# Performance work log

Measured on AMD Instinct MI355X. Metric: run time of the kernel, lower is better.

## Reference

```python
import jax, jax.numpy as jnp
import numpy as np

NUM_HEADS = 12

def setup_inputs() -> dict:
    key = jax.random.key(0)
    ks = jax.random.split(key, 6)
    B, N, C = 4, 2048, 768
    s = 0.02
    return {
        "x": jax.random.normal(ks[0], (B, N, C), jnp.float32),
        "y": jax.random.normal(ks[1], (B, N, C), jnp.float32),
        "Wq": jax.random.normal(ks[2], (C, C), jnp.float32) * s,
        "Wkv": jax.random.normal(ks[3], (2 * C, C), jnp.float32) * s,
        "tau_param": jnp.asarray(1.0, jnp.float32),
        "Wproj": jax.random.normal(ks[4], (C, C), jnp.float32) * s,
        "bproj": jnp.zeros((C,), jnp.float32),
    }

def reference(x, y, Wq, Wkv, tau_param, Wproj, bproj):
    B, N, C = x.shape
    H = NUM_HEADS
    D = C // H
    scale = D ** -0.5
    # q: [B,H,N,D]
    q = (x @ Wq.T).reshape(B, N, H, D).transpose(0, 2, 1, 3) * scale
    kv = (y @ Wkv.T).reshape(B, N, 2, H, D).transpose(2, 0, 3, 1, 4)
    k, v = kv[0], kv[1]
    tau = jax.nn.softplus(tau_param) + 1e-6
    attn = jnp.einsum("bhnd,bhmd->bhnm", q, k) / tau  # [B,H,N,N]
    attn = jax.nn.softmax(attn, axis=-1)
    out = jnp.einsum("bhnm,bhmd->bhnd", attn, v)  # [B,H,N,D]
    out = out.transpose(0, 2, 1, 3).reshape(B, N, C)
    return out @ Wproj.T + bproj
```

## Files before the change

### kernel.cpp

```cpp
#include <hip/hip_runtime.h>
#include <math.h>

typedef unsigned short u16;
typedef unsigned int u32;
typedef __fp16 fp16x2 __attribute__((ext_vector_type(2)));
typedef _Float16 half8 __attribute__((ext_vector_type(8)));
typedef float f32x4 __attribute__((ext_vector_type(4)));

#define NH   12
#define SEQ  2048
#define CDIM 768

__device__ __forceinline__ u16 f2h(float f) {
  _Float16 h = (_Float16)f;
  return __builtin_bit_cast(u16, h);
}
__device__ __forceinline__ u32 pk2(float a, float b) {
  fp16x2 h = __builtin_amdgcn_cvt_pkrtz(a, b);
  return __builtin_bit_cast(u32, h);
}
__device__ __forceinline__ void dma16(const u16* g, u16* l) {
  __builtin_amdgcn_global_load_lds(
      (const __attribute__((address_space(1))) u32*)g,
      (__attribute__((address_space(3))) u32*)l, 16, 0, 0);
}

__global__ __launch_bounds__(256) void cvt_f32_f16(const float* __restrict__ in,
                                                   u16* __restrict__ out, int n) {
  int i = (blockIdx.x * 256 + threadIdx.x) * 4;
  if (i < n) {
    float4 f = *(const float4*)(in + i);
    *(uint2*)(out + i) = make_uint2(pk2(f.x, f.y), pk2(f.z, f.w));
  }
}
__global__ __launch_bounds__(256) void cvt_f32_f16_scale(const float* __restrict__ in,
                                                         u16* __restrict__ out,
                                                         const float* __restrict__ taup, int n) {
  float t = *taup;
  float sp = (t > 20.f) ? t : log1pf(expf(t));
  float s = (0.125f / (sp + 1e-6f)) * 1.44269504088896340736f;
  int i = (blockIdx.x * 256 + threadIdx.x) * 4;
  if (i < n) {
    float4 f = *(const float4*)(in + i);
    *(uint2*)(out + i) = make_uint2(pk2(f.x * s, f.y * s), pk2(f.z * s, f.w * s));
  }
}

template<int MODE>
__global__ __launch_bounds__(128, 3) void gemm_nt(
    const u16* __restrict__ A, const u16* __restrict__ B,
    u16* __restrict__ out0, u16* __restrict__ out1,
    float* __restrict__ outf, const float* __restrict__ bias,
    int M, int N, int K)
{
  __shared__ __align__(16) u16 As[64 * 64];
  __shared__ __align__(16) u16 Bs[128 * 64];
  const int tid = threadIdx.x;
  const int wave = tid >> 6, lane = tid & 63;
  const int quad = lane >> 4, l16 = lane & 15;
  const int row0 = blockIdx.x * 64, col0 = blockIdx.y * 128;

  const int sub = lane >> 3;
  const int csw = ((lane & 7) ^ sub) * 8;

  f32x4 acc[4][4] = {};

  for (int k0 = 0; k0 < K; k0 += 64) {
    __syncthreads();
    #pragma unroll
    for (int i = 0; i < 4; i++) {
      int ii = wave * 4 + i;
      dma16(A + (size_t)(row0 + ii * 8 + sub) * K + k0 + csw, &As[ii * 512]);
    }
    #pragma unroll
    for (int i = 0; i < 8; i++) {
      int ii = wave * 8 + i;
      dma16(B + (size_t)(col0 + ii * 8 + sub) * K + k0 + csw, &Bs[ii * 512]);
    }
    __syncthreads();
    #pragma unroll
    for (int ks = 0; ks < 2; ks++) {
      half8 af[4], bfr[4];
      #pragma unroll
      for (int mt = 0; mt < 4; mt++)
        af[mt] = *(const half8*)&As[(mt * 16 + l16) * 64 + (((ks * 4 + quad) ^ (l16 & 7)) * 8)];
      #pragma unroll
      for (int nt = 0; nt < 4; nt++)
        bfr[nt] = *(const half8*)&Bs[(wave * 64 + nt * 16 + l16) * 64 + (((ks * 4 + quad) ^ (l16 & 7)) * 8)];
      #pragma unroll
      for (int mt = 0; mt < 4; mt++)
        #pragma unroll
        for (int nt = 0; nt < 4; nt++)
          acc[mt][nt] = __builtin_amdgcn_mfma_f32_16x16x32_f16(af[mt], bfr[nt], acc[mt][nt], 0, 0, 0);
    }
  }

  #pragma unroll
  for (int mt = 0; mt < 4; mt++)
  #pragma unroll
  for (int nt = 0; nt < 4; nt++)
  #pragma unroll
  for (int r = 0; r < 4; r++) {
    int gm = row0 + mt * 16 + quad * 4 + r;
    int gn = col0 + wave * 64 + nt * 16 + l16;
    float v = acc[mt][nt][r];
    if (MODE == 0) {
      int b = gm >> 11, n = gm & 2047;
      int h = gn >> 6, d = gn & 63;
      out0[(((size_t)(b * NH + h)) * SEQ + n) * 64 + d] = f2h(v);
    } else if (MODE == 1) {
      int b = gm >> 11, n = gm & 2047;
      if (gn < CDIM) {
        int h = gn >> 6, d = gn & 63;
        out0[(((size_t)(b * NH + h)) * SEQ + n) * 64 + d] = f2h(v);
      } else {
        int c = gn - CDIM;
        int h = c >> 6, d = c & 63;
        out1[(((size_t)(b * NH + h)) * 64 + d) * SEQ + n] = f2h(v);
      }
    } else {
      outf[(size_t)gm * N + gn] = v + bias[gn];
    }
  }
}

__global__ __launch_bounds__(256, 3) void attn_kernel(
    const u16* __restrict__ Q, const u16* __restrict__ Kb,
    const u16* __restrict__ Vtg, u16* __restrict__ Ob)
{
  constexpr int LDP = 72;
  __shared__ __align__(16) u16 Ks[64 * 64];
  __shared__ __align__(16) u16 Vs[64 * 64];
  __shared__ __align__(16) u16 Ps[4 * 16 * LDP];

  const int qt = blockIdx.x & 15;
  const int bh = blockIdx.x >> 4;
  const int b = bh / NH, h = bh % NH;
  const u16* Qp = Q   + (size_t)bh * SEQ * 64;
  const u16* Kp = Kb  + (size_t)bh * SEQ * 64;
  const u16* Vp = Vtg + (size_t)bh * 64 * SEQ;

  const int tid = threadIdx.x;
  const int wave = tid >> 6, lane = tid & 63;
  const int quad = lane >> 4, l16 = lane & 15;
  const int sub = lane >> 3;
  const int csw = ((lane & 7) ^ sub) * 8;
  u16* Pw = Ps + wave * 16 * LDP;

  half8 qf[2][2];
  #pragma unroll
  for (int mt = 0; mt < 2; mt++)
    #pragma unroll
    for (int ks = 0; ks < 2; ks++)
      qf[mt][ks] = *(const half8*)(Qp + (size_t)(qt * 128 + wave * 32 + mt * 16 + l16) * 64 + ks * 32 + quad * 8);

  f32x4 oacc[2][4] = {};
  float lrow[2] = {0.f, 0.f};

  for (int kt = 0; kt < SEQ / 64; kt++) {
    __syncthreads();
    #pragma unroll
    for (int i = 0; i < 2; i++) {
      int ii = wave * 2 + i;
      dma16(Kp + (size_t)(kt * 64 + ii * 8 + sub) * 64 + csw, &Ks[ii * 512]);
      dma16(Vp + (size_t)(ii * 8 + sub) * SEQ + kt * 64 + csw, &Vs[ii * 512]);
    }
    __syncthreads();

    f32x4 sacc[2][4] = {};
    #pragma unroll
    for (int ks = 0; ks < 2; ks++) {
      #pragma unroll
      for (int ntk = 0; ntk < 4; ntk++) {
        half8 kf = *(const half8*)&Ks[(ntk * 16 + l16) * 64 + (((ks * 4 + quad) ^ (l16 & 7)) * 8)];
        #pragma unroll
        for (int mt = 0; mt < 2; mt++)
          sacc[mt][ntk] = __builtin_amdgcn_mfma_f32_16x16x32_f16(kf, qf[mt][ks], sacc[mt][ntk], 0, 0, 0);
      }
    }

    half8 pf[2][2];
    #pragma unroll
    for (int mt = 0; mt < 2; mt++) {
      #pragma unroll
      for (int ntk = 0; ntk < 4; ntk++) {
        float p0 = exp2f(sacc[mt][ntk][0]);
        float p1 = exp2f(sacc[mt][ntk][1]);
        float p2 = exp2f(sacc[mt][ntk][2]);
        float p3 = exp2f(sacc[mt][ntk][3]);
        lrow[mt] += (p0 + p1) + (p2 + p3);
        *(uint2*)(&Pw[l16 * LDP + ntk * 16 + quad * 4]) = make_uint2(pk2(p0, p1), pk2(p2, p3));
      }
      pf[mt][0] = *(const half8*)&Pw[l16 * LDP + quad * 8];
      pf[mt][1] = *(const half8*)&Pw[l16 * LDP + 32 + quad * 8];
    }

    #pragma unroll
    for (int ks = 0; ks < 2; ks++)
      #pragma unroll
      for (int dt = 0; dt < 4; dt++) {
        half8 vf = *(const half8*)&Vs[(dt * 16 + l16) * 64 + (((ks * 4 + quad) ^ (l16 & 7)) * 8)];
        #pragma unroll
        for (int mt = 0; mt < 2; mt++)
          oacc[mt][dt] = __builtin_amdgcn_mfma_f32_16x16x32_f16(pf[mt][ks], vf, oacc[mt][dt], 0, 0, 0);
      }
  }

  #pragma unroll
  for (int mt = 0; mt < 2; mt++) {
    lrow[mt] += __shfl_xor(lrow[mt], 16);
    lrow[mt] += __shfl_xor(lrow[mt], 32);
  }

  #pragma unroll
  for (int mt = 0; mt < 2; mt++) {
    float lv[4];
    #pragma unroll
    for (int r = 0; r < 4; r++) lv[r] = __shfl(lrow[mt], quad * 4 + r);
    #pragma unroll
    for (int r = 0; r < 4; r++) {
      float inv = 1.0f / lv[r];
      int n = qt * 128 + wave * 32 + mt * 16 + quad * 4 + r;
      size_t base = ((size_t)b * SEQ + n) * CDIM + h * 64;
      #pragma unroll
      for (int dt = 0; dt < 4; dt++)
        Ob[base + dt * 16 + l16] = f2h(oacc[mt][dt][r] * inv);
    }
  }
}

extern "C" void kernel_launch(void* const* d_in, const int* in_sizes, int n_in,
                              void* d_out, int out_size, void* d_ws, size_t ws_size,
                              hipStream_t stream)
{
  const float* x     = (const float*)d_in[0];
  const float* y     = (const float*)d_in[1];
  const float* Wq    = (const float*)d_in[2];
  const float* Wkv   = (const float*)d_in[3];
  const float* taup  = (const float*)d_in[4];
  const float* Wproj = (const float*)d_in[5];
  const float* bproj = (const float*)d_in[6];
  float* out = (float*)d_out;

  char* ws = (char*)d_ws;
  size_t off = 0;
  auto alloc = [&](size_t bytes) { char* p = ws + off; off += bytes; return p; };
  u16* xh  = (u16*)alloc(8192ull * 768 * 2);
  u16* yh  = (u16*)alloc(8192ull * 768 * 2);
  u16* wqh = (u16*)alloc(768ull * 768 * 2);
  u16* wkh = (u16*)alloc(1536ull * 768 * 2);
  u16* wph = (u16*)alloc(768ull * 768 * 2);
  u16* qb  = (u16*)alloc(8192ull * 768 * 2);
  u16* kb  = (u16*)alloc(8192ull * 768 * 2);
  u16* vtb = (u16*)alloc(8192ull * 768 * 2);
  u16* ao  = (u16*)alloc(8192ull * 768 * 2);

  cvt_f32_f16<<<6144, 256, 0, stream>>>(x, xh, 8192 * 768);
  cvt_f32_f16<<<6144, 256, 0, stream>>>(y, yh, 8192 * 768);
  cvt_f32_f16_scale<<<576, 256, 0, stream>>>(Wq, wqh, taup, 768 * 768);
  cvt_f32_f16<<<1152, 256, 0, stream>>>(Wkv, wkh, 1536 * 768);
  cvt_f32_f16<<<576, 256, 0, stream>>>(Wproj, wph, 768 * 768);

  gemm_nt<0><<<dim3(128, 6), 128, 0, stream>>>(xh, wqh, qb, nullptr, nullptr, nullptr, 8192, 768, 768);
  gemm_nt<1><<<dim3(128, 12), 128, 0, stream>>>(yh, wkh, kb, vtb, nullptr, nullptr, 8192, 1536, 768);
  attn_kernel<<<dim3(48 * 16), 256, 0, stream>>>(qb, kb, vtb, ao);
  gemm_nt<2><<<dim3(128, 6), 128, 0, stream>>>(ao, wph, nullptr, nullptr, out, bproj, 8192, 768, 768);
}
```

Before: 265.2 us.

## Merge conversion and QKV launches, shrink attention and proj tiles for more blocks

Merges five fp32->fp16 conversion kernels into one launch and fuses the Q and KV projection GEMMs into a single grid. It halves the attention block to 128 threads covering 64 query rows, doubling the grid to 1536 blocks, and runs the output projection with 64-wide N tiles for 1536 blocks. The goal is less launch overhead and better CU fill on the many-CU device. In exchange, the smaller tiles mean each K/V tile is loaded by more blocks, so there is less data reuse per block.

```diff
diff --git a/kernel.cpp b/kernel.cpp
--- a/kernel.cpp
+++ b/kernel.cpp
@@ -25,45 +25,58 @@
       (__attribute__((address_space(3))) u32*)l, 16, 0, 0);
 }
 
-__global__ __launch_bounds__(256) void cvt_f32_f16(const float* __restrict__ in,
-                                                   u16* __restrict__ out, int n) {
-  int i = (blockIdx.x * 256 + threadIdx.x) * 4;
-  if (i < n) {
-    float4 f = *(const float4*)(in + i);
-    *(uint2*)(out + i) = make_uint2(pk2(f.x, f.y), pk2(f.z, f.w));
-  }
-}
-__global__ __launch_bounds__(256) void cvt_f32_f16_scale(const float* __restrict__ in,
-                                                         u16* __restrict__ out,
-                                                         const float* __restrict__ taup, int n) {
-  float t = *taup;
-  float sp = (t > 20.f) ? t : log1pf(expf(t));
-  float s = (0.125f / (sp + 1e-6f)) * 1.44269504088896340736f;
-  int i = (blockIdx.x * 256 + threadIdx.x) * 4;
-  if (i < n) {
-    float4 f = *(const float4*)(in + i);
-    *(uint2*)(out + i) = make_uint2(pk2(f.x * s, f.y * s), pk2(f.z * s, f.w * s));
-  }
-}
-
-template<int MODE>
-__global__ __launch_bounds__(128, 3) void gemm_nt(
-    const u16* __restrict__ A, const u16* __restrict__ B,
-    u16* __restrict__ out0, u16* __restrict__ out1,
-    float* __restrict__ outf, const float* __restrict__ bias,
-    int M, int N, int K)
-{
+__global__ __launch_bounds__(256) void cvt_all(
+    const float* __restrict__ x, const float* __restrict__ y,
+    const float* __restrict__ Wq, const float* __restrict__ Wkv,
+    const float* __restrict__ Wp, const float* __restrict__ taup,
+    u16* __restrict__ xh, u16* __restrict__ yh, u16* __restrict__ wqh,
+    u16* __restrict__ wkh, u16* __restrict__ wph)
+{
+  int blk = blockIdx.x;
+  const float* src; u16* dst; int base; float s = 1.0f;
+  if (blk < 6144)       { src = x;   dst = xh;  base = blk; }
+  else if (blk < 12288) { src = y;   dst = yh;  base = blk - 6144; }
+  else if (blk < 12864) {
+    float t = *taup;
+    float sp = (t > 20.f) ? t : log1pf(expf(t));
+    s = (0.125f / (sp + 1e-6f)) * 1.44269504088896340736f;
+    src = Wq; dst = wqh; base = blk - 12288;
+  }
+  else if (blk < 14016) { src = Wkv; dst = wkh; base = blk - 12864; }
+  else                  { src = Wp;  dst = wph; base = blk - 14016; }
+  int i = (base * 256 + threadIdx.x) * 4;
+  float4 f = *(const float4*)(src + i);
+  *(uint2*)(dst + i) = make_uint2(pk2(f.x * s, f.y * s), pk2(f.z * s, f.w * s));
+}
+
+template<int KIND, int TN>
+__global__ __launch_bounds__(128, 3) void gemm64(
+    const u16* __restrict__ A0, const u16* __restrict__ B0,
+    const u16* __restrict__ A1, const u16* __restrict__ B1,
+    u16* __restrict__ oq, u16* __restrict__ ok, u16* __restrict__ ov,
+    float* __restrict__ outf, const float* __restrict__ bias)
+{
+  constexpr int K = 768;
+  constexpr int NT = TN / 32;
   __shared__ __align__(16) u16 As[64 * 64];
-  __shared__ __align__(16) u16 Bs[128 * 64];
+  __shared__ __align__(16) u16 Bs[TN * 64];
   const int tid = threadIdx.x;
   const int wave = tid >> 6, lane = tid & 63;
   const int quad = lane >> 4, l16 = lane & 15;
-  const int row0 = blockIdx.x * 64, col0 = blockIdx.y * 128;
-
-  const int sub = lane >> 3;
-  const int csw = ((lane & 7) ^ sub) * 8;
-
-  f32x4 acc[4][4] = {};
+  const int row0 = blockIdx.x * 64;
+  const int sub = lane >> 3, csw = ((lane & 7) ^ sub) * 8;
+  const int wn = wave * (TN / 2);
+
+  const u16* A; const u16* B; int col0; bool isQ = true;
+  if (KIND == 0) {
+    int yb = blockIdx.y;
+    if (yb < 6) { A = A0; B = B0; col0 = yb * 128; }
+    else        { A = A1; B = B1; col0 = (yb - 6) * 128; isQ = false; }
+  } else {
+    A = A0; B = B0; col0 = blockIdx.y * TN;
+  }
+
+  f32x4 acc[4][NT] = {};
 
   for (int k0 = 0; k0 < K; k0 += 64) {
     __syncthreads();
@@ -73,68 +86,67 @@
       dma16(A + (size_t)(row0 + ii * 8 + sub) * K + k0 + csw, &As[ii * 512]);
     }
     #pragma unroll
-    for (int i = 0; i < 8; i++) {
-      int ii = wave * 8 + i;
+    for (int i = 0; i < TN / 16; i++) {
+      int ii = wave * (TN / 16) + i;
       dma16(B + (size_t)(col0 + ii * 8 + sub) * K + k0 + csw, &Bs[ii * 512]);
     }
     __syncthreads();
     #pragma unroll
     for (int ks = 0; ks < 2; ks++) {
-      half8 af[4], bfr[4];
+      half8 af[4], bf[NT];
       #pragma unroll
       for (int mt = 0; mt < 4; mt++)
         af[mt] = *(const half8*)&As[(mt * 16 + l16) * 64 + (((ks * 4 + quad) ^ (l16 & 7)) * 8)];
       #pragma unroll
-      for (int nt = 0; nt < 4; nt++)
-        bfr[nt] = *(const half8*)&Bs[(wave * 64 + nt * 16 + l16) * 64 + (((ks * 4 + quad) ^ (l16 & 7)) * 8)];
+      for (int nt = 0; nt < NT; nt++)
+        bf[nt] = *(const half8*)&Bs[(wn + nt * 16 + l16) * 64 + (((ks * 4 + quad) ^ (l16 & 7)) * 8)];
       #pragma unroll
       for (int mt = 0; mt < 4; mt++)
         #pragma unroll
-        for (int nt = 0; nt < 4; nt++)
-          acc[mt][nt] = __builtin_amdgcn_mfma_f32_16x16x32_f16(af[mt], bfr[nt], acc[mt][nt], 0, 0, 0);
+        for (int nt = 0; nt < NT; nt++)
+          acc[mt][nt] = __builtin_amdgcn_mfma_f32_16x16x32_f16(af[mt], bf[nt], acc[mt][nt], 0, 0, 0);
     }
   }
 
   #pragma unroll
   for (int mt = 0; mt < 4; mt++)
   #pragma unroll
-  for (int nt = 0; nt < 4; nt++)
+  for (int nt = 0; nt < NT; nt++)
   #pragma unroll
   for (int r = 0; r < 4; r++) {
     int gm = row0 + mt * 16 + quad * 4 + r;
-    int gn = col0 + wave * 64 + nt * 16 + l16;
+    int gn = col0 + wn + nt * 16 + l16;
     float v = acc[mt][nt][r];
-    if (MODE == 0) {
+    if (KIND == 0) {
       int b = gm >> 11, n = gm & 2047;
-      int h = gn >> 6, d = gn & 63;
-      out0[(((size_t)(b * NH + h)) * SEQ + n) * 64 + d] = f2h(v);
-    } else if (MODE == 1) {
-      int b = gm >> 11, n = gm & 2047;
-      if (gn < CDIM) {
+      if (isQ) {
         int h = gn >> 6, d = gn & 63;
-        out0[(((size_t)(b * NH + h)) * SEQ + n) * 64 + d] = f2h(v);
+        oq[(((size_t)(b * NH + h)) * SEQ + n) * 64 + d] = f2h(v);
+      } else if (gn < CDIM) {
+        int h = gn >> 6, d = gn & 63;
+        ok[(((size_t)(b * NH + h)) * SEQ + n) * 64 + d] = f2h(v);
       } else {
         int c = gn - CDIM;
         int h = c >> 6, d = c & 63;
-        out1[(((size_t)(b * NH + h)) * 64 + d) * SEQ + n] = f2h(v);
+        ov[(((size_t)(b * NH + h)) * 64 + d) * SEQ + n] = f2h(v);
       }
     } else {
-      outf[(size_t)gm * N + gn] = v + bias[gn];
-    }
-  }
-}
-
-__global__ __launch_bounds__(256, 3) void attn_kernel(
+      outf[(size_t)gm * CDIM + gn] = v + bias[gn];
+    }
+  }
+}
+
+__global__ __launch_bounds__(128, 3) void attn_kernel(
     const u16* __restrict__ Q, const u16* __restrict__ Kb,
     const u16* __restrict__ Vtg, u16* __restrict__ Ob)
 {
   constexpr int LDP = 72;
   __shared__ __align__(16) u16 Ks[64 * 64];
   __shared__ __align__(16) u16 Vs[64 * 64];
-  __shared__ __align__(16) u16 Ps[4 * 16 * LDP];
-
-  const int qt = blockIdx.x & 15;
-  const int bh = blockIdx.x >> 4;
+  __shared__ __align__(16) u16 Ps[2 * 16 * LDP];
+
+  const int qt = blockIdx.x & 31;
+  const int bh = blockIdx.x >> 5;
   const int b = bh / NH, h = bh % NH;
   const u16* Qp = Q   + (size_t)bh * SEQ * 64;
   const u16* Kp = Kb  + (size_t)bh * SEQ * 64;
@@ -152,7 +164,7 @@
   for (int mt = 0; mt < 2; mt++)
     #pragma unroll
     for (int ks = 0; ks < 2; ks++)
-      qf[mt][ks] = *(const half8*)(Qp + (size_t)(qt * 128 + wave * 32 + mt * 16 + l16) * 64 + ks * 32 + quad * 8);
+      qf[mt][ks] = *(const half8*)(Qp + (size_t)(qt * 64 + wave * 32 + mt * 16 + l16) * 64 + ks * 32 + quad * 8);
 
   f32x4 oacc[2][4] = {};
   float lrow[2] = {0.f, 0.f};
@@ -160,8 +172,8 @@
   for (int kt = 0; kt < SEQ / 64; kt++) {
     __syncthreads();
     #pragma unroll
-    for (int i = 0; i < 2; i++) {
-      int ii = wave * 2 + i;
+    for (int i = 0; i < 4; i++) {
+      int ii = wave * 4 + i;
       dma16(Kp + (size_t)(kt * 64 + ii * 8 + sub) * 64 + csw, &Ks[ii * 512]);
       dma16(Vp + (size_t)(ii * 8 + sub) * SEQ + kt * 64 + csw, &Vs[ii * 512]);
     }
@@ -220,7 +232,7 @@
     #pragma unroll
     for (int r = 0; r < 4; r++) {
       float inv = 1.0f / lv[r];
-      int n = qt * 128 + wave * 32 + mt * 16 + quad * 4 + r;
+      int n = qt * 64 + wave * 32 + mt * 16 + quad * 4 + r;
       size_t base = ((size_t)b * SEQ + n) * CDIM + h * 64;
       #pragma unroll
       for (int dt = 0; dt < 4; dt++)
@@ -255,14 +267,8 @@
   u16* vtb = (u16*)alloc(8192ull * 768 * 2);
   u16* ao  = (u16*)alloc(8192ull * 768 * 2);
 
-  cvt_f32_f16<<<6144, 256, 0, stream>>>(x, xh, 8192 * 768);
-  cvt_f32_f16<<<6144, 256, 0, stream>>>(y, yh, 8192 * 768);
-  cvt_f32_f16_scale<<<576, 256, 0, stream>>>(Wq, wqh, taup, 768 * 768);
-  cvt_f32_f16<<<1152, 256, 0, stream>>>(Wkv, wkh, 1536 * 768);
-  cvt_f32_f16<<<576, 256, 0, stream>>>(Wproj, wph, 768 * 768);
-
-  gemm_nt<0><<<dim3(128, 6), 128, 0, stream>>>(xh, wqh, qb, nullptr, nullptr, nullptr, 8192, 768, 768);
-  gemm_nt<1><<<dim3(128, 12), 128, 0, stream>>>(yh, wkh, kb, vtb, nullptr, nullptr, 8192, 1536, 768);
-  attn_kernel<<<dim3(48 * 16), 256, 0, stream>>>(qb, kb, vtb, ao);
-  gemm_nt<2><<<dim3(128, 6), 128, 0, stream>>>(ao, wph, nullptr, nullptr, out, bproj, 8192, 768, 768);
-}
+  cvt_all<<<14592, 256, 0, stream>>>(x, y, Wq, Wkv, Wproj, taup, xh, yh, wqh, wkh, wph);
+  gemm64<0, 128><<<dim3(128, 18), 128, 0, stream>>>(xh, wqh, yh, wkh, qb, kb, vtb, nullptr, nullptr);
+  attn_kernel<<<dim3(48 * 32), 128, 0, stream>>>(qb, kb, vtb, ao);
+  gemm64<1, 64><<<dim3(128, 12), 128, 0, stream>>>(ao, wph, nullptr, nullptr, nullptr, nullptr, nullptr, out, bproj);
+}
```

Result: slower. 275.2 us (+3.8%).
